# Performance work log

Hardware: AMD Instinct MI355X
Metric: run time of the kernel (lower is better)

## Reference

```python
import jax, jax.numpy as jnp
import numpy as np

N_NODES = 100000
N_EDGES = 3200000
IN_CH = 128
OUT_CH = 10


def setup_inputs() -> dict:
    key = jax.random.key(0)
    k1, k2, k3 = jax.random.split(key, 3)
    x = jax.random.normal(k1, (N_NODES, IN_CH), dtype=jnp.float32)
    edge_index = jax.random.randint(k2, (2, N_EDGES), 0, N_NODES, dtype=jnp.int64)
    # Glorot-style init for the GCN linear weight, zero bias (PyG defaults)
    W = jax.random.normal(k3, (IN_CH, OUT_CH), dtype=jnp.float32) * (1.0 / np.sqrt(IN_CH))
    b = jnp.zeros((OUT_CH,), dtype=jnp.float32)
    return {"x": x, "edge_index": edge_index, "W": W, "b": b}


def reference(x, edge_index, W, b):
    # GCNConv with default settings: add self-loops, symmetric normalization,
    # linear transform, scatter-add aggregation, then bias.
    n = x.shape[0]
    loops = jnp.arange(n, dtype=edge_index.dtype)
    src = jnp.concatenate([edge_index[0], loops])  # message sources (x_j)
    dst = jnp.concatenate([edge_index[1], loops])  # aggregation targets

    ones = jnp.ones_like(dst, dtype=x.dtype)
    deg = jax.ops.segment_sum(ones, dst, num_segments=n)  # in-degree incl. self-loop
    dinv = jnp.where(deg > 0, jax.lax.rsqrt(deg), 0.0)
    norm = dinv[src] * dinv[dst]  # [E+N]

    xw = x @ W  # [N, OUT_CH] small GEMM before propagation (PyG order)
    msgs = norm[:, None] * xw[src]  # gather + scale, [E+N, OUT_CH]
    out = jax.ops.segment_sum(msgs, dst, num_segments=n)  # scatter-add
    return out + b
```

## Files before the change

kernel.cpp:

```cpp
#include <hip/hip_runtime.h>

#define IN_CH 128
#define OUT_CH 10
#define SHIFT 10
#define NPB 1024
#define CHUNK_C 2048
#define CHUNK_F 4096
#define CCAP 2048
#define DSPL 8
#define OVFCAP (1 << 20)

__device__ __forceinline__ unsigned pk2(float a, float b) {
    unsigned ua = __float_as_uint(a);
    ua = (ua + 0x7fffu + ((ua >> 16) & 1u)) >> 16;
    unsigned ub = __float_as_uint(b);
    ub = (ub + 0x7fffu + ((ub >> 16) & 1u)) >> 16;
    return ua | (ub << 16);
}
__device__ __forceinline__ float lo16(unsigned u) {
    return __uint_as_float(u << 16);
}
__device__ __forceinline__ float hi16(unsigned u) {
    return __uint_as_float(u & 0xffff0000u);
}

__device__ __forceinline__ int load_dst(const void* ei, bool is32, long long E,
                                        long long i) {
    return is32 ? ((const int*)ei)[E + i] : (int)((const long long*)ei)[E + i];
}
__device__ __forceinline__ int load_src(const void* ei, bool is32, long long E,
                                        long long i) {
    return is32 ? ((const int*)ei)[i] : (int)((const long long*)ei)[i];
}


__global__ void k_init_cap(const unsigned int* __restrict__ w,
                           int* __restrict__ gcur, int* __restrict__ bbase,
                           int* __restrict__ ovfcnt, int* __restrict__ flag,
                           int NB, int cap, int nwords_check) {
    __shared__ int any_nz;
    int tid = threadIdx.x;
    for (int i = tid; i < NB; i += 256) {
        gcur[i] = i * cap;
        bbase[i] = i * cap;
    }
    if (tid == 0) {
        any_nz = 0;
        *ovfcnt = 0;
    }
    __syncthreads();
    int local = 0;
    for (int i = tid; i < nwords_check; i += 256)
        if (w[2 * i + 1] != 0u) local = 1;
    if (local) atomicOr(&any_nz, 1);
    __syncthreads();
    if (tid == 0) *flag = any_nz;
}

__global__ void k_init_exact(const unsigned int* __restrict__ w,
                             int* __restrict__ bcnt, int* __restrict__ flag,
                             int NB, int nwords_check) {
    __shared__ int any_nz;
    for (int i = threadIdx.x; i < NB; i += 256) bcnt[i] = 0;
    if (threadIdx.x == 0) any_nz = 0;
    __syncthreads();
    int local = 0;
    for (int i = threadIdx.x; i < nwords_check; i += 256)
        if (w[2 * i + 1] != 0u) local = 1;
    if (local) atomicOr(&any_nz, 1);
    __syncthreads();
    if (threadIdx.x == 0) *flag = any_nz;
}

__global__ void k_zero_i(int* __restrict__ p, int n) {
    int i = blockIdx.x * blockDim.x + threadIdx.x;
    int stride = gridDim.x * blockDim.x;
    for (; i < n; i += stride) p[i] = 0;
}


__global__ void k_bincount(const void* __restrict__ ei,
                           const int* __restrict__ flag, int E,
                           int* __restrict__ bcnt, int NB) {
    __shared__ int h[128];
    for (int i = threadIdx.x; i < NB; i += blockDim.x) h[i] = 0;
    __syncthreads();
    const bool is32 = (*flag != 0);
    long long base = (long long)blockIdx.x * CHUNK_C;
    int lim = (int)min((long long)CHUNK_C, (long long)E - base);
    for (int i = threadIdx.x; i < lim; i += blockDim.x) {
        int d = load_dst(ei, is32, E, base + i);
        atomicAdd(&h[d >> SHIFT], 1);
    }
    __syncthreads();
    for (int i = threadIdx.x; i < NB; i += blockDim.x)
        if (h[i]) atomicAdd(&bcnt[i], h[i]);
}

__global__ void k_scanNB(const int* __restrict__ bcnt, int* __restrict__ bbase,
                         int* __restrict__ gcur, int NB) {
    __shared__ int s[128];
    int tid = threadIdx.x;
    int v = (tid < NB) ? bcnt[tid] : 0;
    if (tid < 128) s[tid] = v;
    __syncthreads();
    for (int off = 1; off < 128; off <<= 1) {
        int t = (tid < 128 && tid >= off) ? s[tid - off] : 0;
        __syncthreads();
        if (tid < 128) s[tid] += t;
        __syncthreads();
    }
    if (tid < NB) {
        int e = s[tid] - v;
        bbase[tid] = e;
        gcur[tid] = e;
    }
}


__global__ void k_binfill(const void* __restrict__ ei,
                          const int* __restrict__ flag, int E,
                          int* __restrict__ gcur, int* __restrict__ pairs,
                          int NB, int cap, int2* __restrict__ ovf,
                          int* __restrict__ ovfcnt) {
    __shared__ int h[128];
    __shared__ int cur[128];
    int tid = threadIdx.x;
    for (int i = tid; i < NB; i += 512) h[i] = 0;
    __syncthreads();
    const bool is32 = (*flag != 0);
    long long base = (long long)blockIdx.x * CHUNK_F;
    int lim = (int)min((long long)CHUNK_F, (long long)E - base);

    int ss[8], dd[8];
#pragma unroll
    for (int j = 0; j < 8; ++j) {
        int i = tid + j * 512;
        if (i < lim) {
            ss[j] = load_src(ei, is32, E, base + i);
            dd[j] = load_dst(ei, is32, E, base + i);
        }
    }
#pragma unroll
    for (int j = 0; j < 8; ++j) {
        int i = tid + j * 512;
        if (i < lim) atomicAdd(&h[dd[j] >> SHIFT], 1);
    }
    __syncthreads();
    for (int i = tid; i < NB; i += 512)
        cur[i] = h[i] ? atomicAdd(&gcur[i], h[i]) : 0;
    __syncthreads();
#pragma unroll
    for (int j = 0; j < 8; ++j) {
        int i = tid + j * 512;
        if (i < lim) {
            int bk = dd[j] >> SHIFT;
            int slot = atomicAdd(&cur[bk], 1);
            if (cap > 0 && slot >= (bk + 1) * cap) {
                int o = atomicAdd(ovfcnt, 1);
                if (o < OVFCAP) {
                    ovf[o].x = ss[j];
                    ovf[o].y = dd[j];
                }
            } else {
                pairs[slot] = (int)(((unsigned)ss[j] << SHIFT) |
                                    (unsigned)(dd[j] & (NPB - 1)));
            }
        }
    }
}

__global__ void k_fin(const int* __restrict__ gcur, int* __restrict__ bcnt,
                      int NB, int cap) {
    int i = threadIdx.x;
    if (i < NB) {
        int c = gcur[i] - i * cap;
        bcnt[i] = c > cap ? cap : c;
    }
}


__global__ void k_deg_part(const int* __restrict__ pairs,
                           const int* __restrict__ bbase,
                           const int* __restrict__ bcnt,
                           int* __restrict__ pdeg) {
    __shared__ int hist[NPB];
    int tid = threadIdx.x;
    for (int j = tid; j < NPB; j += 512) hist[j] = 0;
    __syncthreads();
    int b = blockIdx.x >> 3;
    int s = blockIdx.x & 7;
    int beg = bbase[b], c = bcnt[b];
    int lo = beg + (int)(((long long)c * s) >> 3);
    int hi = beg + (int)(((long long)c * (s + 1)) >> 3);
    for (int i = lo + tid; i < hi; i += 512)
        atomicAdd(&hist[((unsigned)pairs[i]) & (NPB - 1)], 1);
    __syncthreads();
    int* dst = pdeg + (size_t)blockIdx.x * NPB;
    for (int j = tid; j < NPB; j += 512) dst[j] = hist[j];
}

__global__ void k_ovf_deg(const int2* __restrict__ ovf,
                          const int* __restrict__ ovfcnt,
                          int* __restrict__ pdeg) {
    int cnt = *ovfcnt;
    if (cnt > OVFCAP) cnt = OVFCAP;
    int stride = gridDim.x * blockDim.x;
    for (int i = blockIdx.x * blockDim.x + threadIdx.x; i < cnt; i += stride) {
        int d = ovf[i].y;
        int b = d >> SHIFT;
        atomicAdd(&pdeg[((size_t)b * DSPL) * NPB + (d & (NPB - 1))], 1);
    }
}

__global__ void k_xw(const float* __restrict__ x, const float* __restrict__ W,
                     const int* __restrict__ pdeg, float* __restrict__ dinv,
                     unsigned* __restrict__ yw, int N) {
    __shared__ float Wt[OUT_CH][IN_CH];
    for (int i = threadIdx.x; i < IN_CH * OUT_CH; i += blockDim.x) {
        int k = i / OUT_CH, c = i - k * OUT_CH;
        Wt[c][k] = W[i];
    }
    __syncthreads();

    int n = blockIdx.x * blockDim.x + threadIdx.x;
    if (n >= N) return;

    float acc[OUT_CH];
#pragma unroll
    for (int c = 0; c < OUT_CH; ++c) acc[c] = 0.0f;

    const float4* xr = (const float4*)(x + (size_t)n * IN_CH);
#pragma unroll 4
    for (int k4 = 0; k4 < IN_CH / 4; ++k4) {
        float4 xv = xr[k4];
#pragma unroll
        for (int c = 0; c < OUT_CH; ++c) {
            float4 wv = *(const float4*)&Wt[c][k4 * 4];
            acc[c] += xv.x * wv.x + xv.y * wv.y + xv.z * wv.z + xv.w * wv.w;
        }
    }

    int b = n >> SHIFT, l = n & (NPB - 1);
    const int* pd = pdeg + ((size_t)b * DSPL) * NPB + l;
    int deg = 0;
#pragma unroll
    for (int s = 0; s < DSPL; ++s) deg += pd[(size_t)s * NPB];
    float d = rsqrtf(1.0f + (float)deg);
    dinv[n] = d;

    uint4 w0;
    w0.x = pk2(d * acc[0], d * acc[1]);
    w0.y = pk2(d * acc[2], d * acc[3]);
    w0.z = pk2(d * acc[4], d * acc[5]);
    w0.w = pk2(d * acc[6], d * acc[7]);
    *(uint4*)(yw + (size_t)n * 8) = w0;
    yw[(size_t)n * 8 + 4] = pk2(d * acc[8], d * acc[9]);
}

__global__ void k_accum(const int* __restrict__ pairs,
                        const int* __restrict__ bbase,
                        const int* __restrict__ bcnt,
                        const unsigned* __restrict__ yw,
                        float* __restrict__ part) {
    __shared__ int hist[NPB];
    __shared__ int base[NPB];
    __shared__ int cur[NPB];
    __shared__ unsigned sorted[CCAP];
    __shared__ int wsums[8];

    int tid = threadIdx.x;
    int lane = tid & 63;
    int wid = tid >> 6;
    int b = blockIdx.x >> 3;
    int s = blockIdx.x & 7;
    int beg = bbase[b];
    int c = bcnt[b];
    int lo = beg + (int)(((long long)c * s) >> 3);
    int hi = beg + (int)(((long long)c * (s + 1)) >> 3);

    int r0 = tid * 2;

    float acc[2][OUT_CH];
#pragma unroll
    for (int j = 0; j < 2; ++j)
#pragma unroll
        for (int k = 0; k < OUT_CH; ++k) acc[j][k] = 0.0f;

    for (int clo = lo; clo < hi; clo += CCAP) {
        int m = min(CCAP, hi - clo);

        hist[r0] = 0;
        hist[r0 + 1] = 0;
        __syncthreads();

        unsigned mine[4];
#pragma unroll
        for (int j = 0; j < 4; ++j) {
            int i = tid + j * 512;
            if (i < m) {
                unsigned pp = (unsigned)pairs[clo + i];
                mine[j] = pp;
                atomicAdd(&hist[pp & (NPB - 1)], 1);
            }
        }
        __syncthreads();

        int lsum = hist[r0] + hist[r0 + 1];
        int incl = lsum;
#pragma unroll
        for (int off = 1; off < 64; off <<= 1) {
            int t = __shfl_up(incl, off);
            if (lane >= off) incl += t;
        }
        if (lane == 63) wsums[wid] = incl;
        __syncthreads();
        int run = incl - lsum;
        for (int w = 0; w < wid; ++w) run += wsums[w];
        base[r0] = run;
        cur[r0] = run;
        run += hist[r0];
        base[r0 + 1] = run;
        cur[r0 + 1] = run;
        __syncthreads();

#pragma unroll
        for (int j = 0; j < 4; ++j) {
            int i = tid + j * 512;
            if (i < m) {
                unsigned pp = mine[j];
                int slot = atomicAdd(&cur[pp & (NPB - 1)], 1);
                sorted[slot] = pp >> SHIFT;
            }
        }
        __syncthreads();

#pragma unroll
        for (int j = 0; j < 2; ++j) {
            int rb = base[r0 + j];
            int rl = hist[r0 + j];
            for (int q = 0; q < rl; ++q) {
                unsigned src = sorted[rb + q];
                const unsigned* yr = yw + (size_t)src * 8;
                uint4 a = *(const uint4*)yr;
                unsigned w4 = yr[4];
                acc[j][0] += lo16(a.x); acc[j][1] += hi16(a.x);
                acc[j][2] += lo16(a.y); acc[j][3] += hi16(a.y);
                acc[j][4] += lo16(a.z); acc[j][5] += hi16(a.z);
                acc[j][6] += lo16(a.w); acc[j][7] += hi16(a.w);
                acc[j][8] += lo16(w4);  acc[j][9] += hi16(w4);
            }
        }
        __syncthreads();
    }

    float* dst = part + (size_t)blockIdx.x * (NPB * OUT_CH) +
                 (size_t)r0 * OUT_CH;
#pragma unroll
    for (int j = 0; j < 2; ++j)
#pragma unroll
        for (int k = 0; k < OUT_CH; ++k) dst[j * OUT_CH + k] = acc[j][k];
}

__global__ void k_merge(const float* __restrict__ part,
                        const unsigned* __restrict__ yw,
                        const float* __restrict__ dinv,
                        const float* __restrict__ bias,
                        float* __restrict__ out, int N) {
    int idx = blockIdx.x * blockDim.x + threadIdx.x;
    if (idx >= N * OUT_CH) return;
    int n = idx / OUT_CH;
    int ch = idx - n * OUT_CH;
    int b = n >> SHIFT;
    int local = (n & (NPB - 1)) * OUT_CH + ch;
    size_t bs = (size_t)b << 3;
    float s = 0.0f;
#pragma unroll
    for (int q = 0; q < 8; ++q)
        s += part[(bs + q) * (size_t)(NPB * OUT_CH) + local];
    unsigned w = yw[(size_t)n * 8 + (ch >> 1)];
    float yv = (ch & 1) ? hi16(w) : lo16(w);
    out[idx] = dinv[n] * (s + yv) + bias[ch];
}

__global__ void k_ovf_msg(const int2* __restrict__ ovf,
                          const int* __restrict__ ovfcnt,
                          const unsigned* __restrict__ yw,
                          const float* __restrict__ dinv,
                          float* __restrict__ out) {
    int cnt = *ovfcnt;
    if (cnt > OVFCAP) cnt = OVFCAP;
    int stride = gridDim.x * blockDim.x;
    for (int i = blockIdx.x * blockDim.x + threadIdx.x; i < cnt; i += stride) {
        int s = ovf[i].x;
        int d = ovf[i].y;
        float dn = dinv[d];
        const unsigned* yr = yw + (size_t)s * 8;
        uint4 a = *(const uint4*)yr;
        unsigned w4 = yr[4];
        float* orow = out + (size_t)d * OUT_CH;
        atomicAdd(&orow[0], dn * lo16(a.x));
        atomicAdd(&orow[1], dn * hi16(a.x));
        atomicAdd(&orow[2], dn * lo16(a.y));
        atomicAdd(&orow[3], dn * hi16(a.y));
        atomicAdd(&orow[4], dn * lo16(a.z));
        atomicAdd(&orow[5], dn * hi16(a.z));
        atomicAdd(&orow[6], dn * lo16(a.w));
        atomicAdd(&orow[7], dn * hi16(a.w));
        atomicAdd(&orow[8], dn * lo16(w4));
        atomicAdd(&orow[9], dn * hi16(w4));
    }
}


__global__ void k_detect_fb(const unsigned int* __restrict__ w, int* flag,
                            int nwords_check) {
    __shared__ int any_nz;
    if (threadIdx.x == 0) any_nz = 0;
    __syncthreads();
    int local = 0;
    for (int i = threadIdx.x; i < nwords_check; i += blockDim.x)
        if (w[2 * i + 1] != 0u) local = 1;
    if (local) atomicOr(&any_nz, 1);
    __syncthreads();
    if (threadIdx.x == 0) *flag = any_nz;
}

__global__ void k_count_fb(const void* __restrict__ ei, int* __restrict__ cnt,
                           const int* __restrict__ flag, int E) {
    const bool is32 = (*flag != 0);
    long long i = (long long)blockIdx.x * blockDim.x + threadIdx.x;
    long long stride = (long long)gridDim.x * blockDim.x;
    for (; i < E; i += stride) atomicAdd(&cnt[load_dst(ei, is32, E, i)], 1);
}

__global__ void k_xw_fb(const float* __restrict__ x,
                        const float* __restrict__ W,
                        const int* __restrict__ cnt, float* __restrict__ dinv,
                        float* __restrict__ y, float* __restrict__ out_seed,
                        int N) {
    __shared__ float Wt[OUT_CH][IN_CH];
    for (int i = threadIdx.x; i < IN_CH * OUT_CH; i += blockDim.x) {
        int k = i / OUT_CH, c = i - k * OUT_CH;
        Wt[c][k] = W[i];
    }
    __syncthreads();
    int n = blockIdx.x * blockDim.x + threadIdx.x;
    if (n >= N) return;
    float acc[OUT_CH];
#pragma unroll
    for (int c = 0; c < OUT_CH; ++c) acc[c] = 0.0f;
    const float4* xr = (const float4*)(x + (size_t)n * IN_CH);
#pragma unroll 4
    for (int k4 = 0; k4 < IN_CH / 4; ++k4) {
        float4 xv = xr[k4];
#pragma unroll
        for (int c = 0; c < OUT_CH; ++c) {
            float4 wv = *(const float4*)&Wt[c][k4 * 4];
            acc[c] += xv.x * wv.x + xv.y * wv.y + xv.z * wv.z + xv.w * wv.w;
        }
    }
    float d = rsqrtf(1.0f + (float)cnt[n]);
    dinv[n] = d;
    float2* yr = (float2*)(y + (size_t)n * OUT_CH);
    float2* orow = (float2*)(out_seed + (size_t)n * OUT_CH);
#pragma unroll
    for (int c2 = 0; c2 < OUT_CH / 2; ++c2) {
        float2 v;
        v.x = d * acc[2 * c2];
        v.y = d * acc[2 * c2 + 1];
        yr[c2] = v;
        orow[c2] = v;
    }
}

__global__ void k_scatter_fb(const void* __restrict__ ei,
                             const float* __restrict__ y,
                             float* __restrict__ out,
                             const int* __restrict__ flag, int E) {
    const bool is32 = (*flag != 0);
    long long i = (long long)blockIdx.x * blockDim.x + threadIdx.x;
    long long stride = (long long)gridDim.x * blockDim.x;
    for (; i < E; i += stride) {
        long long s = load_src(ei, is32, E, i);
        long long t = load_dst(ei, is32, E, i);
        const float2* yr = (const float2*)(y + s * OUT_CH);
        float2 v0 = yr[0], v1 = yr[1], v2 = yr[2], v3 = yr[3], v4 = yr[4];
        float* orow = out + t * OUT_CH;
        atomicAdd(&orow[0], v0.x);
        atomicAdd(&orow[1], v0.y);
        atomicAdd(&orow[2], v1.x);
        atomicAdd(&orow[3], v1.y);
        atomicAdd(&orow[4], v2.x);
        atomicAdd(&orow[5], v2.y);
        atomicAdd(&orow[6], v3.x);
        atomicAdd(&orow[7], v3.y);
        atomicAdd(&orow[8], v4.x);
        atomicAdd(&orow[9], v4.y);
    }
}

__global__ void k_final_fb(const float* __restrict__ dinv,
                           const float* __restrict__ b,
                           float* __restrict__ out, int N) {
    int n = blockIdx.x * blockDim.x + threadIdx.x;
    if (n >= N) return;
    float d = dinv[n];
    float2* orow = (float2*)(out + (size_t)n * OUT_CH);
#pragma unroll
    for (int c2 = 0; c2 < OUT_CH / 2; ++c2) {
        float2 v = orow[c2];
        v.x = v.x * d + b[2 * c2];
        v.y = v.y * d + b[2 * c2 + 1];
        orow[c2] = v;
    }
}


extern "C" void kernel_launch(void* const* d_in, const int* in_sizes, int n_in,
                              void* d_out, int out_size, void* d_ws,
                              size_t ws_size, hipStream_t stream) {
    const float* x = (const float*)d_in[0];
    const void* ei = d_in[1];
    const float* W = (const float*)d_in[2];
    const float* b = (const float*)d_in[3];
    float* out = (float*)d_out;

    int N = in_sizes[0] / IN_CH;
    int E = in_sizes[1] / 2;

    int NB = (N + NPB - 1) >> SHIFT;
    int nblkN = (N + 255) / 256;
    int nblkC = (E + CHUNK_C - 1) / CHUNK_C;
    int nblkF = (E + CHUNK_F - 1) / CHUNK_F;

    int cap = (E + NB - 1) / NB;
    cap += cap / 4 + 1024;
    cap = (cap + 15) & ~15;

    size_t off_pdeg = 400;
    size_t off_dinv = off_pdeg + (size_t)NB * DSPL * NPB;
    size_t off_yw = (off_dinv + (size_t)N + 15) & ~(size_t)15;
    size_t off_pairs = off_yw + (size_t)8 * N;
    size_t off_ovf = (off_pairs + (size_t)NB * cap + 15) & ~(size_t)15;
    size_t off_part_c = (off_ovf + (size_t)2 * OVFCAP + 15) & ~(size_t)15;
    size_t needed_c = (off_part_c + ((size_t)NB << 3) * (NPB * OUT_CH)) * 4;
    size_t off_part_e = (off_pairs + (size_t)E + 15) & ~(size_t)15;
    size_t needed_e = (off_part_e + ((size_t)NB << 3) * (NPB * OUT_CH)) * 4;

    bool ok_shape = (NB <= 128) && (N <= (1 << 22));

    if (ok_shape && (ws_size >= needed_c || ws_size >= needed_e)) {
        bool use_cap = (ws_size >= needed_c);
        int* wsi = (int*)d_ws;
        int* gcur = wsi;
        int* bbase = wsi + 128;
        int* bcnt = wsi + 256;
        int* flag = wsi + 384;
        int* ovfcnt = wsi + 385;
        int* pdeg = wsi + off_pdeg;
        float* dinv = (float*)(wsi + off_dinv);
        unsigned* yw = (unsigned*)(wsi + off_yw);
        int* pairs = wsi + off_pairs;
        int2* ovf = (int2*)(wsi + off_ovf);
        float* part = (float*)(wsi + (use_cap ? off_part_c : off_part_e));

        if (use_cap) {
            k_init_cap<<<1, 256, 0, stream>>>((const unsigned int*)ei, gcur,
                                              bbase, ovfcnt, flag, NB, cap,
                                              8192);
            k_binfill<<<nblkF, 512, 0, stream>>>(ei, flag, E, gcur, pairs, NB,
                                                 cap, ovf, ovfcnt);
            k_fin<<<1, 128, 0, stream>>>(gcur, bcnt, NB, cap);
            k_deg_part<<<NB * DSPL, 512, 0, stream>>>(pairs, bbase, bcnt,
                                                      pdeg);
            k_ovf_deg<<<32, 256, 0, stream>>>(ovf, ovfcnt, pdeg);
            k_xw<<<nblkN, 256, 0, stream>>>(x, W, pdeg, dinv, yw, N);
            k_accum<<<NB << 3, 512, 0, stream>>>(pairs, bbase, bcnt, yw, part);
            int mthreads = N * OUT_CH;
            k_merge<<<(mthreads + 255) / 256, 256, 0, stream>>>(part, yw, dinv,
                                                                b, out, N);
            k_ovf_msg<<<32, 256, 0, stream>>>(ovf, ovfcnt, yw, dinv, out);
        } else {
            k_init_exact<<<1, 256, 0, stream>>>((const unsigned int*)ei, bcnt,
                                                flag, NB, 8192);
            k_bincount<<<nblkC, 256, 0, stream>>>(ei, flag, E, bcnt, NB);
            k_scanNB<<<1, 128, 0, stream>>>(bcnt, bbase, gcur, NB);
            k_binfill<<<nblkF, 512, 0, stream>>>(ei, flag, E, gcur, pairs, NB,
                                                 0, nullptr, nullptr);
            k_deg_part<<<NB * DSPL, 512, 0, stream>>>(pairs, bbase, bcnt,
                                                      pdeg);
            k_xw<<<nblkN, 256, 0, stream>>>(x, W, pdeg, dinv, yw, N);
            k_accum<<<NB << 3, 512, 0, stream>>>(pairs, bbase, bcnt, yw, part);
            int mthreads = N * OUT_CH;
            k_merge<<<(mthreads + 255) / 256, 256, 0, stream>>>(part, yw, dinv,
                                                                b, out, N);
        }
    } else {
        int* wsi = (int*)d_ws;
        int* cnt = wsi;
        int* flag = cnt + N;
        size_t off = ((size_t)N + 2) & ~(size_t)1;
        float* dinv = (float*)(wsi + off);
        float* y = dinv + N;

        k_zero_i<<<nblkN, 256, 0, stream>>>(cnt, N);
        k_detect_fb<<<1, 256, 0, stream>>>((const unsigned int*)ei, flag,
                                           8192);
        k_count_fb<<<4096, 256, 0, stream>>>(ei, cnt, flag, E);
        k_xw_fb<<<nblkN, 256, 0, stream>>>(x, W, cnt, dinv, y, out, N);
        k_scatter_fb<<<4096, 256, 0, stream>>>(ei, y, out, flag, E);
        k_final_fb<<<nblkN, 256, 0, stream>>>(dinv, b, out, N);
    }
}
```

Measured before the change: 116.2 us.

## Store accumulator partials as bf16, raise bucket split to 16, drop k_fin

Partial sums from k_accum are now packed to bf16 pairs, which halves the partial buffer. The freed space allows a 16-way split per bucket instead of 8, so k_accum launches twice as many blocks. k_merge now processes channel pairs and writes float2. The k_fin launch is removed by computing bucket counts inline from gcur and bbase, and the overflow kernels use fewer blocks. Rounding the partials to bf16 adds precision loss, and the merge must read more partial slices per node.

```diff
diff --git a/kernel.cpp b/kernel.cpp
--- a/kernel.cpp
+++ b/kernel.cpp
@@ -170,27 +170,26 @@
     }
 }
 
-__global__ void k_fin(const int* __restrict__ gcur, int* __restrict__ bcnt,
-                      int NB, int cap) {
-    int i = threadIdx.x;
-    if (i < NB) {
-        int c = gcur[i] - i * cap;
-        bcnt[i] = c > cap ? cap : c;
-    }
+__device__ __forceinline__ int bucket_cnt(const int* gcur, const int* bbase,
+                                          int b, int cap) {
+    int c = gcur[b] - bbase[b];
+    if (cap > 0 && c > cap) c = cap;
+    return c;
 }
 
 
 __global__ void k_deg_part(const int* __restrict__ pairs,
                            const int* __restrict__ bbase,
-                           const int* __restrict__ bcnt,
-                           int* __restrict__ pdeg) {
+                           const int* __restrict__ gcur,
+                           int* __restrict__ pdeg, int cap) {
     __shared__ int hist[NPB];
     int tid = threadIdx.x;
     for (int j = tid; j < NPB; j += 512) hist[j] = 0;
     __syncthreads();
     int b = blockIdx.x >> 3;
     int s = blockIdx.x & 7;
-    int beg = bbase[b], c = bcnt[b];
+    int beg = bbase[b];
+    int c = bucket_cnt(gcur, bbase, b, cap);
     int lo = beg + (int)(((long long)c * s) >> 3);
     int hi = beg + (int)(((long long)c * (s + 1)) >> 3);
     for (int i = lo + tid; i < hi; i += 512)
@@ -260,9 +259,9 @@
 
 __global__ void k_accum(const int* __restrict__ pairs,
                         const int* __restrict__ bbase,
-                        const int* __restrict__ bcnt,
+                        const int* __restrict__ gcur,
                         const unsigned* __restrict__ yw,
-                        float* __restrict__ part) {
+                        unsigned* __restrict__ part, int cap, int split_log) {
     __shared__ int hist[NPB];
     __shared__ int base[NPB];
     __shared__ int cur[NPB];
@@ -272,12 +271,12 @@
     int tid = threadIdx.x;
     int lane = tid & 63;
     int wid = tid >> 6;
-    int b = blockIdx.x >> 3;
-    int s = blockIdx.x & 7;
+    int b = blockIdx.x >> split_log;
+    int s = blockIdx.x & ((1 << split_log) - 1);
     int beg = bbase[b];
-    int c = bcnt[b];
-    int lo = beg + (int)(((long long)c * s) >> 3);
-    int hi = beg + (int)(((long long)c * (s + 1)) >> 3);
+    int c = bucket_cnt(gcur, bbase, b, cap);
+    int lo = beg + (int)(((long long)c * s) >> split_log);
+    int hi = beg + (int)(((long long)c * (s + 1)) >> split_log);
 
     int r0 = tid * 2;
 
@@ -354,33 +353,43 @@
         __syncthreads();
     }
 
-    float* dst = part + (size_t)blockIdx.x * (NPB * OUT_CH) +
-                 (size_t)r0 * OUT_CH;
-#pragma unroll
-    for (int j = 0; j < 2; ++j)
-#pragma unroll
-        for (int k = 0; k < OUT_CH; ++k) dst[j * OUT_CH + k] = acc[j][k];
-}
-
-__global__ void k_merge(const float* __restrict__ part,
+    unsigned* dst = part + (size_t)blockIdx.x * (NPB * 5) + (size_t)r0 * 5;
+#pragma unroll
+    for (int j = 0; j < 2; ++j) {
+        dst[j * 5 + 0] = pk2(acc[j][0], acc[j][1]);
+        dst[j * 5 + 1] = pk2(acc[j][2], acc[j][3]);
+        dst[j * 5 + 2] = pk2(acc[j][4], acc[j][5]);
+        dst[j * 5 + 3] = pk2(acc[j][6], acc[j][7]);
+        dst[j * 5 + 4] = pk2(acc[j][8], acc[j][9]);
+    }
+}
+
+__global__ void k_merge(const unsigned* __restrict__ part,
                         const unsigned* __restrict__ yw,
                         const float* __restrict__ dinv,
                         const float* __restrict__ bias,
-                        float* __restrict__ out, int N) {
+                        float* __restrict__ out, int N, int split_log) {
     int idx = blockIdx.x * blockDim.x + threadIdx.x;
-    if (idx >= N * OUT_CH) return;
-    int n = idx / OUT_CH;
-    int ch = idx - n * OUT_CH;
+    if (idx >= N * 5) return;
+    int n = idx / 5;
+    int p = idx - n * 5;
     int b = n >> SHIFT;
-    int local = (n & (NPB - 1)) * OUT_CH + ch;
-    size_t bs = (size_t)b << 3;
-    float s = 0.0f;
-#pragma unroll
-    for (int q = 0; q < 8; ++q)
-        s += part[(bs + q) * (size_t)(NPB * OUT_CH) + local];
-    unsigned w = yw[(size_t)n * 8 + (ch >> 1)];
-    float yv = (ch & 1) ? hi16(w) : lo16(w);
-    out[idx] = dinv[n] * (s + yv) + bias[ch];
+    int l = n & (NPB - 1);
+    int spl = 1 << split_log;
+    size_t slot0 = (size_t)b << split_log;
+    float s0 = 0.0f, s1 = 0.0f;
+    const unsigned* pp = part + slot0 * (NPB * 5) + (size_t)l * 5 + p;
+    for (int q = 0; q < spl; ++q) {
+        unsigned v = pp[(size_t)q * (NPB * 5)];
+        s0 += lo16(v);
+        s1 += hi16(v);
+    }
+    float d = dinv[n];
+    unsigned w = yw[(size_t)n * 8 + p];
+    float2 o;
+    o.x = d * (s0 + lo16(w)) + bias[2 * p];
+    o.y = d * (s1 + hi16(w)) + bias[2 * p + 1];
+    *(float2*)(out + (size_t)n * OUT_CH + 2 * p) = o;
 }
 
 __global__ void k_ovf_msg(const int2* __restrict__ ovf,
@@ -544,14 +553,24 @@
     size_t off_pairs = off_yw + (size_t)8 * N;
     size_t off_ovf = (off_pairs + (size_t)NB * cap + 15) & ~(size_t)15;
     size_t off_part_c = (off_ovf + (size_t)2 * OVFCAP + 15) & ~(size_t)15;
-    size_t needed_c = (off_part_c + ((size_t)NB << 3) * (NPB * OUT_CH)) * 4;
     size_t off_part_e = (off_pairs + (size_t)E + 15) & ~(size_t)15;
-    size_t needed_e = (off_part_e + ((size_t)NB << 3) * (NPB * OUT_CH)) * 4;
+
+    int use_cap = -1, split_log = 0;
+    for (int pass = 0; pass < 2 && use_cap < 0; ++pass) {
+        size_t op = pass == 0 ? off_part_c : off_part_e;
+        for (int sl = 4; sl >= 3; --sl) {
+            size_t needed = (op + ((size_t)NB << sl) * (NPB * 5)) * 4;
+            if (ws_size >= needed) {
+                use_cap = (pass == 0);
+                split_log = sl;
+                break;
+            }
+        }
+    }
 
     bool ok_shape = (NB <= 128) && (N <= (1 << 22));
 
-    if (ok_shape && (ws_size >= needed_c || ws_size >= needed_e)) {
-        bool use_cap = (ws_size >= needed_c);
+    if (ok_shape && use_cap >= 0) {
         int* wsi = (int*)d_ws;
         int* gcur = wsi;
         int* bbase = wsi + 128;
@@ -563,7 +582,8 @@
         unsigned* yw = (unsigned*)(wsi + off_yw);
         int* pairs = wsi + off_pairs;
         int2* ovf = (int2*)(wsi + off_ovf);
-        float* part = (float*)(wsi + (use_cap ? off_part_c : off_part_e));
+        unsigned* part =
+            (unsigned*)(wsi + (use_cap ? off_part_c : off_part_e));
 
         if (use_cap) {
             k_init_cap<<<1, 256, 0, stream>>>((const unsigned int*)ei, gcur,
@@ -571,16 +591,17 @@
                                               8192);
             k_binfill<<<nblkF, 512, 0, stream>>>(ei, flag, E, gcur, pairs, NB,
                                                  cap, ovf, ovfcnt);
-            k_fin<<<1, 128, 0, stream>>>(gcur, bcnt, NB, cap);
-            k_deg_part<<<NB * DSPL, 512, 0, stream>>>(pairs, bbase, bcnt,
-                                                      pdeg);
-            k_ovf_deg<<<32, 256, 0, stream>>>(ovf, ovfcnt, pdeg);
+            k_deg_part<<<NB * DSPL, 512, 0, stream>>>(pairs, bbase, gcur, pdeg,
+                                                      cap);
+            k_ovf_deg<<<16, 256, 0, stream>>>(ovf, ovfcnt, pdeg);
             k_xw<<<nblkN, 256, 0, stream>>>(x, W, pdeg, dinv, yw, N);
-            k_accum<<<NB << 3, 512, 0, stream>>>(pairs, bbase, bcnt, yw, part);
-            int mthreads = N * OUT_CH;
-            k_merge<<<(mthreads + 255) / 256, 256, 0, stream>>>(part, yw, dinv,
-                                                                b, out, N);
-            k_ovf_msg<<<32, 256, 0, stream>>>(ovf, ovfcnt, yw, dinv, out);
+            k_accum<<<NB << split_log, 512, 0, stream>>>(pairs, bbase, gcur,
+                                                         yw, part, cap,
+                                                         split_log);
+            int mthreads = N * 5;
+            k_merge<<<(mthreads + 255) / 256, 256, 0, stream>>>(
+                part, yw, dinv, b, out, N, split_log);
+            k_ovf_msg<<<16, 256, 0, stream>>>(ovf, ovfcnt, yw, dinv, out);
         } else {
             k_init_exact<<<1, 256, 0, stream>>>((const unsigned int*)ei, bcnt,
                                                 flag, NB, 8192);
@@ -588,13 +609,15 @@
             k_scanNB<<<1, 128, 0, stream>>>(bcnt, bbase, gcur, NB);
             k_binfill<<<nblkF, 512, 0, stream>>>(ei, flag, E, gcur, pairs, NB,
                                                  0, nullptr, nullptr);
-            k_deg_part<<<NB * DSPL, 512, 0, stream>>>(pairs, bbase, bcnt,
-                                                      pdeg);
+            k_deg_part<<<NB * DSPL, 512, 0, stream>>>(pairs, bbase, gcur, pdeg,
+                                                      0);
             k_xw<<<nblkN, 256, 0, stream>>>(x, W, pdeg, dinv, yw, N);
-            k_accum<<<NB << 3, 512, 0, stream>>>(pairs, bbase, bcnt, yw, part);
-            int mthreads = N * OUT_CH;
-            k_merge<<<(mthreads + 255) / 256, 256, 0, stream>>>(part, yw, dinv,
-                                                                b, out, N);
+            k_accum<<<NB << split_log, 512, 0, stream>>>(pairs, bbase, gcur,
+                                                         yw, part, 0,
+                                                         split_log);
+            int mthreads = N * 5;
+            k_merge<<<(mthreads + 255) / 256, 256, 0, stream>>>(
+                part, yw, dinv, b, out, N, split_log);
         }
     } else {
         int* wsi = (int*)d_ws;
```

After: 111.1 us. 1.05x faster.
